# Kernel optimization log

Measured on AMD Instinct MI355X. Metric: run time of the kernel, lower is better.

## Reference

```python
import jax, jax.numpy as jnp
import numpy as np

ROPE_BASE = 10000.0
NEG_INF = jnp.finfo(jnp.float32).min


def _rope_tables(T, head_dim):
    inv_freq = 1.0 / (ROPE_BASE ** (jnp.arange(0, head_dim, 2, dtype=jnp.float32) / head_dim))
    t = jnp.arange(T, dtype=jnp.float32)
    freqs = jnp.einsum('i,j->ij', t, inv_freq)          # [T, head_dim/2]
    emb = jnp.concatenate([freqs, freqs], axis=-1)      # [T, head_dim]
    return jnp.cos(emb), jnp.sin(emb)


def _rotate_half(x):
    d = x.shape[-1] // 2
    return jnp.concatenate([-x[..., d:], x[..., :d]], axis=-1)


def setup_inputs() -> dict:
    key = jax.random.key(0)
    ks = jax.random.split(key, 6)
    B, T, C = 2, 2048, 1024
    s = 0.02
    return {
        'x': jax.random.normal(ks[0], (B, T, C), jnp.float32),
        'attn_mask': jnp.ones((B, T), jnp.int32),
        'wq': jax.random.normal(ks[1], (C, C), jnp.float32) * s,
        'wk': jax.random.normal(ks[2], (C, C), jnp.float32) * s,
        'wv': jax.random.normal(ks[3], (C, C), jnp.float32) * s,
        'wo': jax.random.normal(ks[4], (C, C), jnp.float32) * s,
        'bo': jnp.zeros((C,), jnp.float32),
        'is_causal': 1,
    }


def reference(x, attn_mask, wq, wk, wv, wo, bo, is_causal):
    B, T, C = x.shape
    H = 16
    D = C // H

    q = (x @ wq).reshape(B, T, H, D).transpose(0, 2, 1, 3)  # [B,H,T,D]
    k = (x @ wk).reshape(B, T, H, D).transpose(0, 2, 1, 3)
    v = (x @ wv).reshape(B, T, H, D).transpose(0, 2, 1, 3)

    # inline RoPE (self-attention path); note scaling_factor = 1.0 in this branch,
    # faithful to the original module.
    cos, sin = _rope_tables(T, D)            # [T, D]
    cos = cos[None, None]                    # [1,1,T,D]
    sin = sin[None, None]
    q = q * cos + _rotate_half(q) * sin
    k = k * cos + _rotate_half(k) * sin

    scores = jnp.einsum('bhqd,bhkd->bhqk', q, k)  # [B,H,T,T], scale 1.0 w/ RoPE

    # mask union: padding mask (2D attn_mask) OR causal mask
    pad_mask = ~(attn_mask.astype(bool))[:, None, None, :]            # [B,1,1,T]
    causal = jnp.triu(jnp.ones((T, T), bool), k=1)[None, None]        # [1,1,T,T]
    if is_causal:
        final_mask = pad_mask | causal
    else:
        final_mask = pad_mask
    scores = jnp.where(final_mask, NEG_INF, scores)

    attn = jax.nn.softmax(scores, axis=-1)   # dropout omitted (eval mode)
    out = jnp.einsum('bhqk,bhkd->bhqd', attn, v)
    out = out.transpose(0, 2, 1, 3).reshape(B, T, C)
    return out @ wo + bo
```

## Files before the change

### kernel.cpp

```cpp
#include <hip/hip_runtime.h>
#include <hip/hip_bf16.h>
#include <stdint.h>

#define B_ 2
#define T_ 2048
#define C_ 1024
#define H_ 16
#define D_ 64
#define NEG_INF_F (-3.4028234663852886e38f)

typedef __bf16 bf16;
typedef __bf16 bf16x4 __attribute__((ext_vector_type(4)));
typedef __bf16 bf16x8 __attribute__((ext_vector_type(8)));
typedef float  f32x4  __attribute__((ext_vector_type(4)));

__device__ __forceinline__ void gload16(const bf16* g, bf16* l) {
  __builtin_amdgcn_global_load_lds(
      (const __attribute__((address_space(1))) void*)(g),
      (__attribute__((address_space(3))) void*)(l), 16, 0, 0);
}

__device__ __forceinline__ f32x4 mfma16(bf16x8 a, bf16x8 b, f32x4 c) {
  return __builtin_amdgcn_mfma_f32_16x16x32_bf16(a, b, c, 0, 0, 0);
}


__global__ void k_prep_x(const float* __restrict__ x, bf16* __restrict__ xb) {
  int i = (blockIdx.x * 256 + threadIdx.x) * 4;
  float4 v = *(const float4*)(x + i);
  bf16x4 o;
  o[0] = (bf16)v.x; o[1] = (bf16)v.y; o[2] = (bf16)v.z; o[3] = (bf16)v.w;
  *(bf16x4*)(xb + i) = o;
}

__global__ void k_prep_wrm(const float* __restrict__ wq, const float* __restrict__ wk,
                           const float* __restrict__ wv, const float* __restrict__ wo,
                           bf16* __restrict__ wqkvT, bf16* __restrict__ woT,
                           float* __restrict__ rc, float* __restrict__ rs,
                           const int* __restrict__ amask, float* __restrict__ negm,
                           unsigned char* __restrict__ tileclean) {
  __shared__ float tile[32][33];
  const int mat = blockIdx.z;
  const int tid = threadIdx.x;
  if (mat < 4) {
    const float* src = (mat == 0) ? wq : (mat == 1) ? wk : (mat == 2) ? wv : wo;
    bf16* dst = (mat < 3) ? (wqkvT + (size_t)mat * C_ * C_) : woT;
    int k0 = blockIdx.y * 32, n0 = blockIdx.x * 32;
    int tx = tid & 31, ty = tid >> 5;
    #pragma unroll
    for (int r = 0; r < 32; r += 8)
      tile[ty + r][tx] = src[(size_t)(k0 + ty + r) * C_ + n0 + tx];
    __syncthreads();
    #pragma unroll
    for (int r = 0; r < 32; r += 8)
      dst[(size_t)(n0 + ty + r) * C_ + k0 + tx] = (bf16)tile[tx][ty + r];
    return;
  }
  const int flat = blockIdx.y * 32 + blockIdx.x;
  if (flat < 256) {
    int i = flat * 256 + tid;
    int t = i >> 5, d = i & 31;
    float inv = expf(-(float)(2 * d) * (9.210340371976184f / 64.0f));
    float fr = (float)t * inv;
    rc[i] = cosf(fr);
    rs[i] = sinf(fr);
  } else if (flat < 256 + B_) {
    int b = flat - 256;
    int base = b * T_ + tid * 8;
    int4 a0 = *(const int4*)(amask + base);
    int4 a1 = *(const int4*)(amask + base + 4);
    bool ok = a0.x && a0.y && a0.z && a0.w && a1.x && a1.y && a1.z && a1.w;
    float4 f0, f1;
    f0.x = a0.x ? 0.f : NEG_INF_F; f0.y = a0.y ? 0.f : NEG_INF_F;
    f0.z = a0.z ? 0.f : NEG_INF_F; f0.w = a0.w ? 0.f : NEG_INF_F;
    f1.x = a1.x ? 0.f : NEG_INF_F; f1.y = a1.y ? 0.f : NEG_INF_F;
    f1.z = a1.z ? 0.f : NEG_INF_F; f1.w = a1.w ? 0.f : NEG_INF_F;
    *(float4*)(negm + base) = f0;
    *(float4*)(negm + base + 4) = f1;
    unsigned long long m = __ballot(ok);
    int w = tid >> 6, lane = tid & 63;
    if (lane < 8) {
      tileclean[b * 32 + w * 8 + lane] =
          (unsigned char)(((m >> (lane * 8)) & 0xFFull) == 0xFFull);
    }
  }
}

template <int MODE, int BM>
__global__ __launch_bounds__(256, 2)
void k_gemm(const bf16* __restrict__ A, const bf16* __restrict__ BT,
            const float* __restrict__ rc, const float* __restrict__ rs,
            bf16* __restrict__ qb, bf16* __restrict__ kbuf, bf16* __restrict__ vtb,
            const float* __restrict__ bo, float* __restrict__ outp) {
  constexpr int K = C_;
  constexpr int MI = BM / 32;
  __shared__ __align__(16) bf16 lA[BM * 32];
  __shared__ __align__(16) bf16 lB[128 * 32];
  const int tid = threadIdx.x;
  const int m0 = blockIdx.y * BM, n0 = blockIdx.x * 128;
  const int lane = tid & 63, w = tid >> 6;
  const int l15 = lane & 15, g = lane >> 4;
  const int wm = (w >> 1) * (BM / 2), wn = (w & 1) * 64;

  f32x4 acc[MI][4] = {};

  const int srow = tid >> 2;
  const int skb = tid & 3;
  const int scol = ((skb ^ ((srow ^ (srow >> 2)) & 3)) << 3);
  const bf16* gA = A + (size_t)(m0 + srow) * K + scol;
  const bf16* gB = BT + (size_t)(n0 + srow) * K + scol;
  bf16* sA = lA + tid * 8;
  bf16* sB = lB + tid * 8;

  const int fsw = ((l15 ^ (l15 >> 2)) & 3);

  for (int k0 = 0; k0 < K; k0 += 32) {
    gload16(gA + k0, sA);
    if constexpr (BM == 128) gload16(gA + (size_t)64 * K + k0, sA + 2048);
    gload16(gB + k0, sB);
    gload16(gB + (size_t)64 * K + k0, sB + 2048);
    __syncthreads();

    bf16x8 af[MI], bfr[4];
    #pragma unroll
    for (int i = 0; i < MI; i++) {
      int row = wm + i * 16 + l15;
      af[i] = *(const bf16x8*)(lA + row * 32 + ((g ^ fsw) << 3));
    }
    #pragma unroll
    for (int j = 0; j < 4; j++) {
      int rowb = wn + j * 16 + l15;
      bfr[j] = *(const bf16x8*)(lB + rowb * 32 + ((g ^ fsw) << 3));
    }
    #pragma unroll
    for (int i = 0; i < MI; i++)
      #pragma unroll
      for (int j = 0; j < 4; j++)
        acc[i][j] = mfma16(af[i], bfr[j], acc[i][j]);
    __syncthreads();
  }

  if constexpr (MODE == 0) {
    const int region = n0 >> 10;
    const int nr = (n0 & 1023) + wn;
    const int h = nr >> 6;
    if (region < 2) {
      bf16* dst = (region == 0) ? qb : kbuf;
      #pragma unroll
      for (int i = 0; i < MI; i++) {
        #pragma unroll
        for (int r = 0; r < 4; r++) {
          int m = m0 + wm + i * 16 + g * 4 + r;
          int b = m >> 11, t = m & 2047;
          size_t base = ((size_t)(b * H_ + h) * T_ + t) * 64;
          #pragma unroll
          for (int j = 0; j < 2; j++) {
            int dl = j * 16 + l15;
            float c = rc[t * 32 + dl], s = rs[t * 32 + dl];
            float lo = acc[i][j][r], hi = acc[i][j + 2][r];
            dst[base + dl]      = (bf16)(lo * c - hi * s);
            dst[base + dl + 32] = (bf16)(hi * c + lo * s);
          }
        }
      }
    } else {
      #pragma unroll
      for (int i = 0; i < MI; i++)
        #pragma unroll
        for (int j = 0; j < 4; j++) {
          int d = j * 16 + l15;
          #pragma unroll
          for (int r = 0; r < 4; r++) {
            int m = m0 + wm + i * 16 + g * 4 + r;
            int b = m >> 11, t = m & 2047;
            vtb[((size_t)(b * H_ + h) * 64 + d) * T_ + t] = (bf16)acc[i][j][r];
          }
        }
    }
  } else {
    #pragma unroll
    for (int i = 0; i < MI; i++)
      #pragma unroll
      for (int j = 0; j < 4; j++) {
        int n = n0 + wn + j * 16 + l15;
        float bias = bo[n];
        #pragma unroll
        for (int r = 0; r < 4; r++) {
          int m = m0 + wm + i * 16 + g * 4 + r;
          outp[(size_t)m * C_ + n] = acc[i][j][r] + bias;
        }
      }
  }
}

__global__ __launch_bounds__(256, 4)
void k_attn(const bf16* __restrict__ qb, const bf16* __restrict__ kbuf,
            const bf16* __restrict__ vtb, const float* __restrict__ negm,
            const unsigned char* __restrict__ tileclean,
            const int* __restrict__ pcausal, bf16* __restrict__ ob) {
  __shared__ __align__(16) bf16 lK[2][64 * 64];
  __shared__ __align__(16) bf16 lV[2][64 * 64];
  __shared__ __align__(16) bf16 lP[4][16 * 64];
  const int bx = blockIdx.x;
  const int qi = 31 - (bx >> 5);
  const int bh = bx & 31;
  const int b = bh >> 4, h = bh & 15;
  const int causal = pcausal[0];
  const int tid = threadIdx.x, lane = tid & 63, w = tid >> 6;
  const int l15 = lane & 15, g = lane >> 4;
  const int sw7 = l15 & 7;
  const int q0 = qi * 64;
  const int wq0 = q0 + w * 16;
  const size_t plane = (size_t)(b * H_ + h) * T_ * 64;

  const int nkt = causal ? (qi + 1) : (T_ / 64);

  unsigned int bits = 0;
  {
    const unsigned char* tcb = tileclean + b * 32;
    #pragma unroll
    for (int i2 = 0; i2 < 32; i2++) bits |= ((unsigned int)tcb[i2]) << i2;
  }

  bf16x8 qf[2];
  #pragma unroll
  for (int kf = 0; kf < 2; kf++)
    qf[kf] = *(const bf16x8*)(qb + plane + (size_t)(wq0 + l15) * 64 + kf * 32 + g * 8);

  f32x4 o[4] = {};
  float psum[4] = {0.f, 0.f, 0.f, 0.f};

  const int srow = tid >> 3;
  const int skb = tid & 7;
  const int scol = ((skb ^ (srow & 7)) << 3);
  const bf16* gK = kbuf + plane + (size_t)srow * 64 + scol;
  const bf16* gV = vtb + plane + (size_t)srow * T_ + scol;
  bf16* myP = lP[w];

  {
    bf16* sKd = lK[0] + tid * 8;
    bf16* sVd = lV[0] + tid * 8;
    gload16(gK, sKd);
    gload16(gK + (size_t)32 * 64, sKd + 2048);
    gload16(gV, sVd);
    gload16(gV + (size_t)32 * T_, sVd + 2048);
  }
  __syncthreads();

  int cur = 0;
  for (int kt = 0; kt < nkt; kt++) {
    if (kt + 1 < nkt) {
      const size_t nk0 = (size_t)(kt + 1) * 64;
      bf16* sKd = lK[cur ^ 1] + tid * 8;
      bf16* sVd = lV[cur ^ 1] + tid * 8;
      gload16(gK + nk0 * 64, sKd);
      gload16(gK + (nk0 + 32) * 64, sKd + 2048);
      gload16(gV + nk0, sVd);
      gload16(gV + (size_t)32 * T_ + nk0, sVd + 2048);
    }
    __builtin_amdgcn_sched_barrier(0);

    const bf16* cK = lK[cur];
    const bf16* cV = lV[cur];
    const size_t k0 = (size_t)kt * 64;

    f32x4 s[4] = {};
    #pragma unroll
    for (int j = 0; j < 4; j++) {
      const int kr = j * 16 + l15;
      bf16x8 k0f = *(const bf16x8*)(cK + kr * 64 + (((0 + g) ^ sw7) << 3));
      bf16x8 k1f = *(const bf16x8*)(cK + kr * 64 + (((4 + g) ^ sw7) << 3));
      s[j] = mfma16(qf[0], k0f, s[j]);
      s[j] = mfma16(qf[1], k1f, s[j]);
    }

    if (!((bits >> kt) & 1)) {
      #pragma unroll
      for (int j = 0; j < 4; j++) {
        float nm = negm[b * T_ + (int)k0 + j * 16 + l15];
        #pragma unroll
        for (int r = 0; r < 4; r++) s[j][r] += nm;
      }
    }
    if (causal && (kt == nkt - 1)) {
      #pragma unroll
      for (int j = 0; j < 4; j++) {
        const int kkg = (int)k0 + j * 16 + l15;
        #pragma unroll
        for (int r = 0; r < 4; r++) {
          const int qg = wq0 + g * 4 + r;
          if (kkg > qg) s[j][r] = NEG_INF_F;
        }
      }
    }

    #pragma unroll
    for (int r = 0; r < 4; r++) {
      float p0 = __expf(s[0][r]), p1 = __expf(s[1][r]);
      float p2 = __expf(s[2][r]), p3 = __expf(s[3][r]);
      s[0][r] = p0; s[1][r] = p1; s[2][r] = p2; s[3][r] = p3;
      psum[r] += (p0 + p1) + (p2 + p3);
    }

    #pragma unroll
    for (int j = 0; j < 4; j++) {
      const int col = j * 16 + l15;
      const int kb2 = col >> 3, c7 = col & 7;
      #pragma unroll
      for (int r = 0; r < 4; r++) {
        const int rw = g * 4 + r;
        myP[rw * 64 + ((kb2 ^ (rw & 7)) << 3) + c7] = (bf16)s[j][r];
      }
    }

    #pragma unroll
    for (int kt2 = 0; kt2 < 2; kt2++) {
      bf16x8 pa = *(const bf16x8*)(myP + l15 * 64 + (((kt2 * 4 + g) ^ sw7) << 3));
      #pragma unroll
      for (int df = 0; df < 4; df++) {
        bf16x8 bv = *(const bf16x8*)(cV + (df * 16 + l15) * 64 + (((kt2 * 4 + g) ^ sw7) << 3));
        o[df] = mfma16(pa, bv, o[df]);
      }
    }

    __syncthreads();
    cur ^= 1;
  }

  float inv[4];
  #pragma unroll
  for (int r = 0; r < 4; r++) {
    float t = psum[r];
    t += __shfl_xor(t, 1);
    t += __shfl_xor(t, 2);
    t += __shfl_xor(t, 4);
    t += __shfl_xor(t, 8);
    inv[r] = 1.0f / t;
  }
  #pragma unroll
  for (int df = 0; df < 4; df++) {
    const int d = df * 16 + l15;
    #pragma unroll
    for (int r = 0; r < 4; r++) {
      const int t = wq0 + g * 4 + r;
      ob[((size_t)(b * T_ + t)) * C_ + h * 64 + d] = (bf16)(o[df][r] * inv[r]);
    }
  }
}

extern "C" void kernel_launch(void* const* d_in, const int* in_sizes, int n_in,
                              void* d_out, int out_size, void* d_ws, size_t ws_size,
                              hipStream_t stream) {
  const float* x  = (const float*)d_in[0];
  const int* amask = (const int*)d_in[1];
  const float* wq = (const float*)d_in[2];
  const float* wk = (const float*)d_in[3];
  const float* wv = (const float*)d_in[4];
  const float* wo = (const float*)d_in[5];
  const float* bo = (const float*)d_in[6];
  const int* isc  = (const int*)d_in[7];
  float* outp = (float*)d_out;

  char* ws = (char*)d_ws;
  bf16* xb    = (bf16*)(ws);
  bf16* wqkvT = (bf16*)(ws + ((size_t)8 << 20));
  bf16* woT   = (bf16*)(ws + ((size_t)14 << 20));
  float* rc   = (float*)(ws + ((size_t)16 << 20));
  float* rs   = (float*)(ws + ((size_t)16 << 20) + (256 << 10));
  float* negm = (float*)(ws + ((size_t)16 << 20) + (512 << 10));
  unsigned char* tileclean = (unsigned char*)(ws + ((size_t)16 << 20) + (528 << 10));
  bf16* qbuf  = (bf16*)(ws + ((size_t)17 << 20));
  bf16* kbuf  = (bf16*)(ws + ((size_t)25 << 20));
  bf16* vtbuf = (bf16*)(ws + ((size_t)33 << 20));
  bf16* obuf  = (bf16*)(ws + ((size_t)41 << 20));

  hipLaunchKernelGGL(k_prep_x, dim3(4096), dim3(256), 0, stream, x, xb);
  hipLaunchKernelGGL(k_prep_wrm, dim3(32, 32, 5), dim3(256), 0, stream,
                     wq, wk, wv, wo, wqkvT, woT, rc, rs, amask, negm, tileclean);
  hipLaunchKernelGGL((k_gemm<0, 128>), dim3(24, 32), dim3(256), 0, stream,
                     xb, wqkvT, rc, rs, qbuf, kbuf, vtbuf, nullptr, nullptr);
  hipLaunchKernelGGL(k_attn, dim3(1024), dim3(256), 0, stream,
                     qbuf, kbuf, vtbuf, negm, tileclean, isc, obuf);
  hipLaunchKernelGGL((k_gemm<1, 64>), dim3(8, 64), dim3(256), 0, stream,
                     obuf, woT, nullptr, nullptr, nullptr, nullptr, nullptr, bo, outp);
}
```

Measured before the change: 185.8 us.

## Double GEMM K-step to 64 and remap blocks for XCD-local L2 reuse

The GEMM kernels now load a 64-wide K slice per iteration, using a new 8-way XOR swizzle. That halves the number of loop iterations and barriers per tile and runs two MFMA sub-steps for each load. The launch grid is flattened to 1D and blocks are remapped so that each XCD (bid&7) handles a contiguous band of M tiles across all N tiles, which should improve L2 hit rates for the shared A rows. LDS use per block doubles, which could limit occupancy under the two-blocks-per-CU launch bound.

```diff
diff --git a/kernel.cpp b/kernel.cpp
--- a/kernel.cpp
+++ b/kernel.cpp
@@ -94,49 +94,55 @@
             const float* __restrict__ bo, float* __restrict__ outp) {
   constexpr int K = C_;
   constexpr int MI = BM / 32;
-  __shared__ __align__(16) bf16 lA[BM * 32];
-  __shared__ __align__(16) bf16 lB[128 * 32];
+  constexpr int NT = (MODE == 0) ? 24 : 8;
+  constexpr int MCH = (MODE == 0) ? 4 : 8;
+  __shared__ __align__(16) bf16 lA[BM * 64];
+  __shared__ __align__(16) bf16 lB[128 * 64];
   const int tid = threadIdx.x;
-  const int m0 = blockIdx.y * BM, n0 = blockIdx.x * 128;
+  const int bid = blockIdx.x;
+  const int xcd = bid & 7, idx = bid >> 3;
+  const int mt = xcd * MCH + idx / NT;
+  const int nt = idx % NT;
+  const int m0 = mt * BM, n0 = nt * 128;
   const int lane = tid & 63, w = tid >> 6;
   const int l15 = lane & 15, g = lane >> 4;
   const int wm = (w >> 1) * (BM / 2), wn = (w & 1) * 64;
 
   f32x4 acc[MI][4] = {};
 
-  const int srow = tid >> 2;
-  const int skb = tid & 3;
-  const int scol = ((skb ^ ((srow ^ (srow >> 2)) & 3)) << 3);
-  const bf16* gA = A + (size_t)(m0 + srow) * K + scol;
-  const bf16* gB = BT + (size_t)(n0 + srow) * K + scol;
+  const int srow = tid >> 3;
+  const int scb = (tid & 7) ^ (srow & 7);
+  const bf16* gA = A + (size_t)(m0 + srow) * K + scb * 8;
+  const bf16* gB = BT + (size_t)(n0 + srow) * K + scb * 8;
   bf16* sA = lA + tid * 8;
   bf16* sB = lB + tid * 8;
-
-  const int fsw = ((l15 ^ (l15 >> 2)) & 3);
-
-  for (int k0 = 0; k0 < K; k0 += 32) {
-    gload16(gA + k0, sA);
-    if constexpr (BM == 128) gload16(gA + (size_t)64 * K + k0, sA + 2048);
-    gload16(gB + k0, sB);
-    gload16(gB + (size_t)64 * K + k0, sB + 2048);
+  const int swl = l15 & 7;
+
+  for (int k0 = 0; k0 < K; k0 += 64) {
+    #pragma unroll
+    for (int i = 0; i < BM / 32; i++)
+      gload16(gA + (size_t)(i * 32) * K + k0, sA + i * 2048);
+    #pragma unroll
+    for (int i = 0; i < 4; i++)
+      gload16(gB + (size_t)(i * 32) * K + k0, sB + i * 2048);
     __syncthreads();
 
-    bf16x8 af[MI], bfr[4];
-    #pragma unroll
-    for (int i = 0; i < MI; i++) {
-      int row = wm + i * 16 + l15;
-      af[i] = *(const bf16x8*)(lA + row * 32 + ((g ^ fsw) << 3));
-    }
-    #pragma unroll
-    for (int j = 0; j < 4; j++) {
-      int rowb = wn + j * 16 + l15;
-      bfr[j] = *(const bf16x8*)(lB + rowb * 32 + ((g ^ fsw) << 3));
-    }
-    #pragma unroll
-    for (int i = 0; i < MI; i++)
+    #pragma unroll
+    for (int kk = 0; kk < 2; kk++) {
+      bf16x8 af[MI], bfr[4];
+      const int pcb = ((kk * 4 + g) ^ swl) << 3;
+      #pragma unroll
+      for (int i = 0; i < MI; i++)
+        af[i] = *(const bf16x8*)(lA + (wm + i * 16 + l15) * 64 + pcb);
       #pragma unroll
       for (int j = 0; j < 4; j++)
-        acc[i][j] = mfma16(af[i], bfr[j], acc[i][j]);
+        bfr[j] = *(const bf16x8*)(lB + (wn + j * 16 + l15) * 64 + pcb);
+      #pragma unroll
+      for (int i = 0; i < MI; i++)
+        #pragma unroll
+        for (int j = 0; j < 4; j++)
+          acc[i][j] = mfma16(af[i], bfr[j], acc[i][j]);
+    }
     __syncthreads();
   }
 
@@ -377,10 +383,10 @@
   hipLaunchKernelGGL(k_prep_x, dim3(4096), dim3(256), 0, stream, x, xb);
   hipLaunchKernelGGL(k_prep_wrm, dim3(32, 32, 5), dim3(256), 0, stream,
                      wq, wk, wv, wo, wqkvT, woT, rc, rs, amask, negm, tileclean);
-  hipLaunchKernelGGL((k_gemm<0, 128>), dim3(24, 32), dim3(256), 0, stream,
+  hipLaunchKernelGGL((k_gemm<0, 128>), dim3(768), dim3(256), 0, stream,
                      xb, wqkvT, rc, rs, qbuf, kbuf, vtbuf, nullptr, nullptr);
   hipLaunchKernelGGL(k_attn, dim3(1024), dim3(256), 0, stream,
                      qbuf, kbuf, vtbuf, negm, tileclean, isc, obuf);
-  hipLaunchKernelGGL((k_gemm<1, 64>), dim3(8, 64), dim3(256), 0, stream,
+  hipLaunchKernelGGL((k_gemm<1, 64>), dim3(512), dim3(256), 0, stream,
                      obuf, woT, nullptr, nullptr, nullptr, nullptr, nullptr, bo, outp);
 }
```

After: 178.4 us. 1.04x faster.
